# Performance work log

Measured on AMD Instinct MI355X. Metric: run time of the kernel, lower is better.

## Reference

```python
import jax, jax.numpy as jnp
import numpy as np

INPUT_DIM = 1024
UNITS = 1024

def setup_inputs() -> dict:
    key = jax.random.key(0)
    ks = jax.random.split(key, 7)
    B, S = 4, 2048
    x = jax.random.normal(ks[0], (B, S, INPUT_DIM), dtype=jnp.float32)
    # nn.Linear weights stored as [out, in]; biases [out]
    scale = 1.0 / np.sqrt(INPUT_DIM)
    Wq = jax.random.uniform(ks[1], (UNITS, INPUT_DIM), jnp.float32, -scale, scale)
    bq = jax.random.uniform(ks[2], (UNITS,), jnp.float32, -scale, scale)
    Wk = jax.random.uniform(ks[3], (UNITS, INPUT_DIM), jnp.float32, -scale, scale)
    bk = jax.random.uniform(ks[4], (UNITS,), jnp.float32, -scale, scale)
    Wv = jax.random.uniform(ks[5], (UNITS, INPUT_DIM), jnp.float32, -scale, scale)
    bv = jax.random.uniform(ks[6], (UNITS,), jnp.float32, -scale, scale)
    return {"x": x, "Wq": Wq, "bq": bq, "Wk": Wk, "bk": bk, "Wv": Wv, "bv": bv}

def reference(x, Wq, bq, Wk, bk, Wv, bv):
    # Q/K/V projections: [B,S,D] @ [D,U]
    Q = jnp.einsum('bsd,ud->bsu', x, Wq) + bq
    K = jnp.einsum('bsd,ud->bsu', x, Wk) + bk
    V = jnp.einsum('bsd,ud->bsu', x, Wv) + bv
    scores = jnp.einsum('bqu,bku->bqk', Q, K) / jnp.sqrt(jnp.float32(UNITS))
    attn = jax.nn.softmax(scores, axis=-1)
    return jnp.einsum('bqk,bku->bqu', attn, V)
```

## Files before the change

kernel.cpp:

```cpp
#include <hip/hip_runtime.h>
#include <cstdint>
#include <cstddef>


typedef unsigned short ushort_t;
typedef __attribute__((ext_vector_type(8))) short short8;
typedef __attribute__((ext_vector_type(4))) float f32x4;

#define AS1 __attribute__((address_space(1)))
#define AS3 __attribute__((address_space(3)))

__device__ __forceinline__ ushort_t f2bf(float f) {
    unsigned int u = __float_as_uint(f);
    u += 0x7FFFu + ((u >> 16) & 1u);
    return (ushort_t)(u >> 16);
}
__device__ __forceinline__ float bf2f(ushort_t b) {
    return __uint_as_float(((unsigned)b) << 16);
}

__device__ __forceinline__ void async_ld16(const void* g, unsigned lds_off) {
    __builtin_amdgcn_global_load_lds((const AS1 void*)(uintptr_t)g,
                                     (AS3 void*)(uintptr_t)lds_off,
                                     16, 0, 0);
}

template <typename OT, int EPI, int CX, int CY>
__global__ __launch_bounds__(256, 2) void gemm_db(
    const ushort_t* __restrict__ A, const ushort_t* __restrict__ B,
    const float* __restrict__ bias0, const float* __restrict__ bias1,
    OT* __restrict__ C, int K, int lda, int ldb, int ldc, float scale,
    long long aOffZ, long long bOffZ, long long cOffZ)
{
    constexpr int BK = 64;
    constexpr int NCALL = 4;

    __shared__ __align__(16) ushort_t As[2][128 * BK];
    __shared__ __align__(16) ushort_t Bs[2][128 * BK];
    __shared__ float rs[128];

    const int tid  = threadIdx.x;
    const int wave = tid >> 6;
    const int lane = tid & 63;

    const int GX  = gridDim.x, GY = gridDim.y, GZ = gridDim.z;
    const int bid = blockIdx.x + GX * (blockIdx.y + GY * blockIdx.z);
    const int xcd = bid & 7;
    const int jj  = bid >> 3;
    const int CZ  = (GX * GY * GZ) / (8 * CX * CY);
    const int NCX = GX / CX, NCY = GY / CY;
    const int cx  = xcd % NCX;
    const int ct  = xcd / NCX;
    const int cy  = ct % NCY, cz = ct / NCY;
    const int bx  = cx * CX + (jj % CX);
    const int by  = cy * CY + ((jj / CX) % CY);
    const int bz  = cz * CZ + jj / (CX * CY);

    A += (size_t)bz * aOffZ;
    B += (size_t)bz * bOffZ;

    const int m0 = by * 128;
    const int n0 = bx * 128;
    const int wm = (wave >> 1) * 64;
    const int wn = (wave & 1) * 64;

    const unsigned lw  = (unsigned)(wave << 10);
    const unsigned aL0 = (unsigned)(uintptr_t)&As[0][0] + lw;
    const unsigned aL1 = (unsigned)(uintptr_t)&As[1][0] + lw;
    const unsigned bL0 = (unsigned)(uintptr_t)&Bs[0][0] + lw;
    const unsigned bL1 = (unsigned)(uintptr_t)&Bs[1][0] + lw;

    const int srow = wave * 8 + (lane >> 3);
    const int cd   = ((lane & 7) - srow) & 7;
    const ushort_t* gA = A + (size_t)(m0 + srow) * lda + cd * 8;
    const ushort_t* gB = B + (size_t)(n0 + srow) * ldb + cd * 8;

    auto stageT = [&](int t, unsigned la, unsigned lb) {
        const ushort_t* pA = gA + (size_t)t * BK;
        const ushort_t* pB = gB + (size_t)t * BK;
#pragma unroll
        for (int c = 0; c < NCALL; ++c) {
            async_ld16(pA + (size_t)(c * 32) * lda, la + c * 4096);
            async_ld16(pB + (size_t)(c * 32) * ldb, lb + c * 4096);
        }
    };

    const int frow = lane & 15;
    const int fg   = lane >> 4;

    const int NT = K / BK;

    f32x4 acc[4][4] = {};
    float rsacc[4] = {0.f, 0.f, 0.f, 0.f};

    auto computeT = [&](const ushort_t* Aw, const ushort_t* Bw) {
#pragma unroll
        for (int t2 = 0; t2 < 2; ++t2) {
            const int pa = (((t2 << 2) + fg + frow) & 7) << 3;
            short8 af[4], bf[4];
#pragma unroll
            for (int i = 0; i < 4; ++i)
                af[i] = *(const short8*)&Aw[(wm + i * 16 + frow) * BK + pa];
            if (EPI == 4 && wn == 0) {
#pragma unroll
                for (int i = 0; i < 4; ++i)
#pragma unroll
                    for (int e = 0; e < 8; ++e)
                        rsacc[i] += bf2f((ushort_t)af[i][e]);
            }
#pragma unroll
            for (int j = 0; j < 4; ++j)
                bf[j] = *(const short8*)&Bw[(wn + j * 16 + frow) * BK + pa];
#pragma unroll
            for (int i = 0; i < 4; ++i)
#pragma unroll
                for (int j = 0; j < 4; ++j)
                    acc[i][j] = __builtin_amdgcn_mfma_f32_16x16x32_bf16(
                        af[i], bf[j], acc[i][j], 0, 0, 0);
        }
    };

    const ushort_t* A0 = &As[0][0];
    const ushort_t* A1 = &As[1][0];
    const ushort_t* B0 = &Bs[0][0];
    const ushort_t* B1 = &Bs[1][0];

    stageT(0, aL0, bL0);
    __syncthreads();

    int t = 0;
    for (; t + 2 < NT; t += 2) {
        stageT(t + 1, aL1, bL1);
        computeT(A0, B0);
        __syncthreads();
        stageT(t + 2, aL0, bL0);
        computeT(A1, B1);
        __syncthreads();
    }
    stageT(NT - 1, aL1, bL1);
    computeT(A0, B0);
    __syncthreads();
    computeT(A1, B1);

    if (EPI == 4) {
        if (wn == 0) {
#pragma unroll
            for (int i = 0; i < 4; ++i) {
                float s = rsacc[i];
                s += __shfl_xor(s, 16, 64);
                s += __shfl_xor(s, 32, 64);
                rs[wm + i * 16 + frow] = s;
            }
        }
        __syncthreads();
    }

    C += (size_t)bz * cOffZ;
    const int r0 = fg << 2;
    const int c0 = lane & 15;
#pragma unroll
    for (int i = 0; i < 4; ++i) {
        float bm[4];
        if (EPI == 2) {
#pragma unroll
            for (int r = 0; r < 4; ++r)
                bm[r] = bias0[m0 + wm + i * 16 + r0 + r];
        }
        if (EPI == 4) {
#pragma unroll
            for (int r = 0; r < 4; ++r)
                bm[r] = 1.0f / rs[wm + i * 16 + r0 + r];
        }
#pragma unroll
        for (int j = 0; j < 4; ++j) {
            const int n = n0 + wn + j * 16 + c0;
            float bn = 0.f;
            if (EPI == 1) bn = (n < 1024) ? bias0[n] : bias1[n - 1024];
#pragma unroll
            for (int r = 0; r < 4; ++r) {
                const int m = m0 + wm + i * 16 + r0 + r;
                float v = acc[i][j][r] * scale;
                if (EPI == 1) v += bn;
                if (EPI == 2) v += bm[r];
                if (EPI == 3) v = __expf(v);
                if (EPI == 4) v *= bm[r];
                if constexpr (sizeof(OT) == 2)
                    C[(size_t)m * ldc + n] = f2bf(v);
                else
                    C[(size_t)m * ldc + n] = v;
            }
        }
    }
}

__global__ __launch_bounds__(256) void cvt_all(
    const float* __restrict__ x,  const float* __restrict__ wq,
    const float* __restrict__ wk, const float* __restrict__ wv,
    ushort_t* __restrict__ xb,  ushort_t* __restrict__ wqb,
    ushort_t* __restrict__ wkb, ushort_t* __restrict__ wvb)
{
    const int b = blockIdx.x;
    const float* src; ushort_t* dst; size_t base;
    if (b < 4096)      { src = x;  dst = xb;  base = (size_t)b * 2048; }
    else if (b < 4608) { src = wq; dst = wqb; base = (size_t)(b - 4096) * 2048; }
    else if (b < 5120) { src = wk; dst = wkb; base = (size_t)(b - 4608) * 2048; }
    else               { src = wv; dst = wvb; base = (size_t)(b - 5120) * 2048; }
    const size_t i = base + threadIdx.x * 8;
    const f32x4 a = *(const f32x4*)(src + i);
    const f32x4 c = *(const f32x4*)(src + i + 4);
    short8 o;
    o[0] = (short)f2bf(a[0]); o[1] = (short)f2bf(a[1]);
    o[2] = (short)f2bf(a[2]); o[3] = (short)f2bf(a[3]);
    o[4] = (short)f2bf(c[0]); o[5] = (short)f2bf(c[1]);
    o[6] = (short)f2bf(c[2]); o[7] = (short)f2bf(c[3]);
    *(short8*)(dst + i) = o;
}

extern "C" void kernel_launch(void* const* d_in, const int* in_sizes, int n_in,
                              void* d_out, int out_size, void* d_ws, size_t ws_size,
                              hipStream_t stream)
{
    const float* x  = (const float*)d_in[0];
    const float* Wq = (const float*)d_in[1];
    const float* bq = (const float*)d_in[2];
    const float* Wk = (const float*)d_in[3];
    const float* bk = (const float*)d_in[4];
    const float* Wv = (const float*)d_in[5];
    const float* bv = (const float*)d_in[6];
    float* out = (float*)d_out;

    char* ws = (char*)d_ws;
    const size_t MB = 1ull << 20;
    ushort_t* Xb   = (ushort_t*)(ws);
    ushort_t* Wqkb = (ushort_t*)(ws + 16 * MB);
    ushort_t* Wvb  = (ushort_t*)(ws + 20 * MB);
    ushort_t* QKb  = (ushort_t*)(ws + 32 * MB);
    ushort_t* Vt   = (ushort_t*)(ws + 64 * MB);
    ushort_t* Sc   = (ushort_t*)(ws);

    cvt_all<<<dim3(5632), dim3(256), 0, stream>>>(
        x, Wq, Wk, Wv, Xb, Wqkb, (ushort_t*)(ws + 18 * MB), Wvb);

    gemm_db<ushort_t, 1, 8, 16><<<dim3(16, 64, 1), dim3(256), 0, stream>>>(
        Xb, Wqkb, bq, bk, QKb, 1024, 1024, 1024, 2048, 1.0f, 0, 0, 0);

    gemm_db<ushort_t, 2, 16, 4><<<dim3(64, 8, 1), dim3(256), 0, stream>>>(
        Wvb, Xb, bv, nullptr, Vt, 1024, 1024, 1024, 8192, 1.0f, 0, 0, 0);

    gemm_db<ushort_t, 3, 8, 16><<<dim3(16, 16, 4), dim3(256), 0, stream>>>(
        QKb, QKb + 1024, nullptr, nullptr, Sc, 1024, 2048, 2048, 2048,
        0.03125f, 2048ll * 2048, 2048ll * 2048, 2048ll * 2048);

    gemm_db<float, 4, 8, 8><<<dim3(8, 16, 4), dim3(256), 0, stream>>>(
        Sc, Vt, nullptr, nullptr, out, 2048, 2048, 8192, 1024, 1.0f,
        2048ll * 2048, 2048ll, 2048ll * 1024);
}
```

Baseline: 239.0 us.

## Merge QK and V projection GEMMs into one launch; compute row sums via MFMA

The separate QK-projection and V-projection GEMM launches become one kernel with 1536 blocks that pick their operands, XCD-aware tile mapping and bias epilogue from the block index. This removes a launch and the tail idle time between the two GEMMs. In the final PV GEMM, the per-row sum of the bf16 attention weights is now computed with an extra MFMA against a vector of ones instead of scalar bf16-to-float adds followed by shuffles. The cost is more MFMA work in wn==0 waves and a larger, branchier merged kernel. An unused remap2 helper is also added.

Measured after the change: 235.3 us. No clear change (-1.6%).

```diff
diff --git a/kernel.cpp b/kernel.cpp
--- a/kernel.cpp
+++ b/kernel.cpp
@@ -15,9 +15,6 @@
     u += 0x7FFFu + ((u >> 16) & 1u);
     return (ushort_t)(u >> 16);
 }
-__device__ __forceinline__ float bf2f(ushort_t b) {
-    return __uint_as_float(((unsigned)b) << 16);
-}
 
 __device__ __forceinline__ void async_ld16(const void* g, unsigned lds_off) {
     __builtin_amdgcn_global_load_lds((const AS1 void*)(uintptr_t)g,
@@ -25,10 +22,20 @@
                                      16, 0, 0);
 }
 
+__device__ __forceinline__ void remap2(int id, int GX, int GY, int CX, int CY,
+                                       int& bx, int& by) {
+    const int xcd = id & 7;
+    const int jj  = id >> 3;
+    const int NCX = GX / CX;
+    const int cx  = xcd % NCX;
+    const int cy  = xcd / NCX;
+    bx = cx * CX + jj % CX;
+    by = cy * CY + (jj / CX) % ((GY / CY) == 0 ? 1 : CY);
+}
+
 template <typename OT, int EPI, int CX, int CY>
 __global__ __launch_bounds__(256, 2) void gemm_db(
     const ushort_t* __restrict__ A, const ushort_t* __restrict__ B,
-    const float* __restrict__ bias0, const float* __restrict__ bias1,
     OT* __restrict__ C, int K, int lda, int ldb, int ldc, float scale,
     long long aOffZ, long long bOffZ, long long cOffZ)
 {
@@ -91,7 +98,10 @@
     const int NT = K / BK;
 
     f32x4 acc[4][4] = {};
-    float rsacc[4] = {0.f, 0.f, 0.f, 0.f};
+    f32x4 rsm[4] = {};
+    const short8 ones = { (short)0x3F80, (short)0x3F80, (short)0x3F80,
+                          (short)0x3F80, (short)0x3F80, (short)0x3F80,
+                          (short)0x3F80, (short)0x3F80 };
 
     auto computeT = [&](const ushort_t* Aw, const ushort_t* Bw) {
 #pragma unroll
@@ -104,9 +114,8 @@
             if (EPI == 4 && wn == 0) {
 #pragma unroll
                 for (int i = 0; i < 4; ++i)
-#pragma unroll
-                    for (int e = 0; e < 8; ++e)
-                        rsacc[i] += bf2f((ushort_t)af[i][e]);
+                    rsm[i] = __builtin_amdgcn_mfma_f32_16x16x32_bf16(
+                        af[i], ones, rsm[i], 0, 0, 0);
             }
 #pragma unroll
             for (int j = 0; j < 4; ++j)
@@ -142,30 +151,24 @@
     __syncthreads();
     computeT(A1, B1);
 
-    if (EPI == 4) {
-        if (wn == 0) {
-#pragma unroll
-            for (int i = 0; i < 4; ++i) {
-                float s = rsacc[i];
-                s += __shfl_xor(s, 16, 64);
-                s += __shfl_xor(s, 32, 64);
-                rs[wm + i * 16 + frow] = s;
-            }
-        }
-        __syncthreads();
-    }
-
-    C += (size_t)bz * cOffZ;
     const int r0 = fg << 2;
     const int c0 = lane & 15;
+
+    if (EPI == 4) {
+        if (wn == 0 && c0 == 0) {
+#pragma unroll
+            for (int i = 0; i < 4; ++i)
+#pragma unroll
+                for (int r = 0; r < 4; ++r)
+                    rs[wm + i * 16 + r0 + r] = rsm[i][r];
+        }
+        __syncthreads();
+    }
+
+    C += (size_t)bz * cOffZ;
 #pragma unroll
     for (int i = 0; i < 4; ++i) {
         float bm[4];
-        if (EPI == 2) {
-#pragma unroll
-            for (int r = 0; r < 4; ++r)
-                bm[r] = bias0[m0 + wm + i * 16 + r0 + r];
-        }
         if (EPI == 4) {
 #pragma unroll
             for (int r = 0; r < 4; ++r)
@@ -174,20 +177,150 @@
 #pragma unroll
         for (int j = 0; j < 4; ++j) {
             const int n = n0 + wn + j * 16 + c0;
-            float bn = 0.f;
-            if (EPI == 1) bn = (n < 1024) ? bias0[n] : bias1[n - 1024];
 #pragma unroll
             for (int r = 0; r < 4; ++r) {
                 const int m = m0 + wm + i * 16 + r0 + r;
                 float v = acc[i][j][r] * scale;
-                if (EPI == 1) v += bn;
-                if (EPI == 2) v += bm[r];
                 if (EPI == 3) v = __expf(v);
                 if (EPI == 4) v *= bm[r];
                 if constexpr (sizeof(OT) == 2)
                     C[(size_t)m * ldc + n] = f2bf(v);
                 else
                     C[(size_t)m * ldc + n] = v;
+            }
+        }
+    }
+}
+
+__global__ __launch_bounds__(256, 2) void gemm_mrg(
+    const ushort_t* __restrict__ Xb, const ushort_t* __restrict__ Wqkb,
+    const ushort_t* __restrict__ Wvb,
+    const float* __restrict__ bq, const float* __restrict__ bk,
+    const float* __restrict__ bv,
+    ushort_t* __restrict__ QKb, ushort_t* __restrict__ Vtp)
+{
+    constexpr int BK = 64;
+    constexpr int NCALL = 4;
+
+    __shared__ __align__(16) ushort_t As[2][128 * BK];
+    __shared__ __align__(16) ushort_t Bs[2][128 * BK];
+
+    const int tid  = threadIdx.x;
+    const int wave = tid >> 6;
+    const int lane = tid & 63;
+
+    const bool vtR = (blockIdx.x >= 1024);
+    const int  id  = vtR ? (int)blockIdx.x - 1024 : (int)blockIdx.x;
+
+    int bx, by;
+    if (!vtR) {
+        const int xcd = id & 7, jj = id >> 3;
+        bx = (xcd % 2) * 8  + (jj % 8);
+        by = (xcd / 2) * 16 + (jj / 8);
+    } else {
+        const int xcd = id & 7, jj = id >> 3;
+        bx = (xcd % 4) * 16 + (jj % 16);
+        by = (xcd / 4) * 4  + (jj / 16);
+    }
+
+    const ushort_t* A = vtR ? Wvb : Xb;
+    const ushort_t* B = vtR ? Xb  : Wqkb;
+    ushort_t*       C = vtR ? Vtp : QKb;
+    const int ldc = vtR ? 8192 : 2048;
+
+    const int m0 = by * 128;
+    const int n0 = bx * 128;
+    const int wm = (wave >> 1) * 64;
+    const int wn = (wave & 1) * 64;
+
+    const unsigned lw  = (unsigned)(wave << 10);
+    const unsigned aL0 = (unsigned)(uintptr_t)&As[0][0] + lw;
+    const unsigned aL1 = (unsigned)(uintptr_t)&As[1][0] + lw;
+    const unsigned bL0 = (unsigned)(uintptr_t)&Bs[0][0] + lw;
+    const unsigned bL1 = (unsigned)(uintptr_t)&Bs[1][0] + lw;
+
+    const int srow = wave * 8 + (lane >> 3);
+    const int cd   = ((lane & 7) - srow) & 7;
+    const ushort_t* gA = A + (size_t)(m0 + srow) * 1024 + cd * 8;
+    const ushort_t* gB = B + (size_t)(n0 + srow) * 1024 + cd * 8;
+
+    auto stageT = [&](int t, unsigned la, unsigned lb) {
+        const ushort_t* pA = gA + (size_t)t * BK;
+        const ushort_t* pB = gB + (size_t)t * BK;
+#pragma unroll
+        for (int c = 0; c < NCALL; ++c) {
+            async_ld16(pA + (size_t)(c * 32) * 1024, la + c * 4096);
+            async_ld16(pB + (size_t)(c * 32) * 1024, lb + c * 4096);
+        }
+    };
+
+    const int frow = lane & 15;
+    const int fg   = lane >> 4;
+
+    f32x4 acc[4][4] = {};
+
+    auto computeT = [&](const ushort_t* Aw, const ushort_t* Bw) {
+#pragma unroll
+        for (int t2 = 0; t2 < 2; ++t2) {
+            const int pa = (((t2 << 2) + fg + frow) & 7) << 3;
+            short8 af[4], bf[4];
+#pragma unroll
+            for (int i = 0; i < 4; ++i)
+                af[i] = *(const short8*)&Aw[(wm + i * 16 + frow) * BK + pa];
+#pragma unroll
+            for (int j = 0; j < 4; ++j)
+                bf[j] = *(const short8*)&Bw[(wn + j * 16 + frow) * BK + pa];
+#pragma unroll
+            for (int i = 0; i < 4; ++i)
+#pragma unroll
+                for (int j = 0; j < 4; ++j)
+                    acc[i][j] = __builtin_amdgcn_mfma_f32_16x16x32_bf16(
+                        af[i], bf[j], acc[i][j], 0, 0, 0);
+        }
+    };
+
+    const ushort_t* A0 = &As[0][0];
+    const ushort_t* A1 = &As[1][0];
+    const ushort_t* B0 = &Bs[0][0];
+    const ushort_t* B1 = &Bs[1][0];
+
+    stageT(0, aL0, bL0);
+    __syncthreads();
+
+    int t = 0;
+    for (; t + 2 < 16; t += 2) {
+        stageT(t + 1, aL1, bL1);
+        computeT(A0, B0);
+        __syncthreads();
+        stageT(t + 2, aL0, bL0);
+        computeT(A1, B1);
+        __syncthreads();
+    }
+    stageT(15, aL1, bL1);
+    computeT(A0, B0);
+    __syncthreads();
+    computeT(A1, B1);
+
+    const int r0 = fg << 2;
+    const int c0 = lane & 15;
+#pragma unroll
+    for (int i = 0; i < 4; ++i) {
+        float bm[4];
+        if (vtR) {
+#pragma unroll
+            for (int r = 0; r < 4; ++r)
+                bm[r] = bv[m0 + wm + i * 16 + r0 + r];
+        }
+#pragma unroll
+        for (int j = 0; j < 4; ++j) {
+            const int n = n0 + wn + j * 16 + c0;
+            float bn = 0.f;
+            if (!vtR) bn = (n < 1024) ? bq[n] : bk[n - 1024];
+#pragma unroll
+            for (int r = 0; r < 4; ++r) {
+                const int m = m0 + wm + i * 16 + r0 + r;
+                float v = acc[i][j][r] + (vtR ? bm[r] : bn);
+                C[(size_t)m * ldc + n] = f2bf(v);
             }
         }
     }
@@ -241,17 +374,14 @@
     cvt_all<<<dim3(5632), dim3(256), 0, stream>>>(
         x, Wq, Wk, Wv, Xb, Wqkb, (ushort_t*)(ws + 18 * MB), Wvb);
 
-    gemm_db<ushort_t, 1, 8, 16><<<dim3(16, 64, 1), dim3(256), 0, stream>>>(
-        Xb, Wqkb, bq, bk, QKb, 1024, 1024, 1024, 2048, 1.0f, 0, 0, 0);
-
-    gemm_db<ushort_t, 2, 16, 4><<<dim3(64, 8, 1), dim3(256), 0, stream>>>(
-        Wvb, Xb, bv, nullptr, Vt, 1024, 1024, 1024, 8192, 1.0f, 0, 0, 0);
+    gemm_mrg<<<dim3(1536), dim3(256), 0, stream>>>(
+        Xb, Wqkb, Wvb, bq, bk, bv, QKb, Vt);
 
     gemm_db<ushort_t, 3, 8, 16><<<dim3(16, 16, 4), dim3(256), 0, stream>>>(
-        QKb, QKb + 1024, nullptr, nullptr, Sc, 1024, 2048, 2048, 2048,
+        QKb, QKb + 1024, Sc, 1024, 2048, 2048, 2048,
         0.03125f, 2048ll * 2048, 2048ll * 2048, 2048ll * 2048);
 
     gemm_db<float, 4, 8, 8><<<dim3(8, 16, 4), dim3(256), 0, stream>>>(
-        Sc, Vt, nullptr, nullptr, out, 2048, 2048, 8192, 1024, 1.0f,
+        Sc, Vt, out, 2048, 2048, 8192, 1024, 1.0f,
         2048ll * 2048, 2048ll, 2048ll * 1024);
 }
```

## Fuse pipeline into cooperative persistent megakernel with grid syncs

Applied to the files above, without the earlier changes.

Replaces the separate cast and GEMM launches with one cooperative persistent kernel that loops over work units and uses grid-wide syncs between stages. This removes per-launch gaps and tail effects. The fallback path merges the QK and V projection GEMMs into a single launch. The softmax row-sum is now computed with an MFMA against a ones vector instead of scalar adds. Risks include grid.sync overhead and the fixed 512-block grid underfilling or imbalancing work across stages.

After: 218.9 us. 1.09x faster.

```diff
diff --git a/kernel.cpp b/kernel.cpp
--- a/kernel.cpp
+++ b/kernel.cpp
@@ -1,6 +1,9 @@
 #include <hip/hip_runtime.h>
+#include <hip/hip_cooperative_groups.h>
 #include <cstdint>
 #include <cstddef>
+
+namespace cg = cooperative_groups;
 
 
 typedef unsigned short ushort_t;
@@ -15,9 +18,6 @@
     u += 0x7FFFu + ((u >> 16) & 1u);
     return (ushort_t)(u >> 16);
 }
-__device__ __forceinline__ float bf2f(ushort_t b) {
-    return __uint_as_float(((unsigned)b) << 16);
-}
 
 __device__ __forceinline__ void async_ld16(const void* g, unsigned lds_off) {
     __builtin_amdgcn_global_load_lds((const AS1 void*)(uintptr_t)g,
@@ -25,42 +25,30 @@
                                      16, 0, 0);
 }
 
-template <typename OT, int EPI, int CX, int CY>
-__global__ __launch_bounds__(256, 2) void gemm_db(
+template <int GX, int GY, int GZ, int CX, int CY>
+__device__ __forceinline__ void remapC(int id, int& bx, int& by, int& bz) {
+    constexpr int CZ  = (GX * GY * GZ) / (8 * CX * CY);
+    constexpr int NCX = GX / CX, NCY = GY / CY;
+    const int xcd = id & 7, jj = id >> 3;
+    const int cx = xcd % NCX, ct = xcd / NCX;
+    const int cy = ct % NCY, cz = ct / NCY;
+    bx = cx * CX + (jj % CX);
+    by = cy * CY + ((jj / CX) % CY);
+    bz = cz * CZ + jj / (CX * CY);
+}
+
+template <typename OT, int EPI>
+__device__ __forceinline__ void gemm_unit(
+    ushort_t (&As)[2][8192], ushort_t (&Bs)[2][8192], float (&rs)[128],
     const ushort_t* __restrict__ A, const ushort_t* __restrict__ B,
-    const float* __restrict__ bias0, const float* __restrict__ bias1,
-    OT* __restrict__ C, int K, int lda, int ldb, int ldc, float scale,
-    long long aOffZ, long long bOffZ, long long cOffZ)
+    const float* __restrict__ b0, const float* __restrict__ b1,
+    OT* __restrict__ C, int NT, int lda, int ldb, int ldc, float scale,
+    int m0, int n0)
 {
     constexpr int BK = 64;
-    constexpr int NCALL = 4;
-
-    __shared__ __align__(16) ushort_t As[2][128 * BK];
-    __shared__ __align__(16) ushort_t Bs[2][128 * BK];
-    __shared__ float rs[128];
-
     const int tid  = threadIdx.x;
     const int wave = tid >> 6;
     const int lane = tid & 63;
-
-    const int GX  = gridDim.x, GY = gridDim.y, GZ = gridDim.z;
-    const int bid = blockIdx.x + GX * (blockIdx.y + GY * blockIdx.z);
-    const int xcd = bid & 7;
-    const int jj  = bid >> 3;
-    const int CZ  = (GX * GY * GZ) / (8 * CX * CY);
-    const int NCX = GX / CX, NCY = GY / CY;
-    const int cx  = xcd % NCX;
-    const int ct  = xcd / NCX;
-    const int cy  = ct % NCY, cz = ct / NCY;
-    const int bx  = cx * CX + (jj % CX);
-    const int by  = cy * CY + ((jj / CX) % CY);
-    const int bz  = cz * CZ + jj / (CX * CY);
-
-    A += (size_t)bz * aOffZ;
-    B += (size_t)bz * bOffZ;
-
-    const int m0 = by * 128;
-    const int n0 = bx * 128;
     const int wm = (wave >> 1) * 64;
     const int wn = (wave & 1) * 64;
 
@@ -79,7 +67,7 @@
         const ushort_t* pA = gA + (size_t)t * BK;
         const ushort_t* pB = gB + (size_t)t * BK;
 #pragma unroll
-        for (int c = 0; c < NCALL; ++c) {
+        for (int c = 0; c < 4; ++c) {
             async_ld16(pA + (size_t)(c * 32) * lda, la + c * 4096);
             async_ld16(pB + (size_t)(c * 32) * ldb, lb + c * 4096);
         }
@@ -88,10 +76,11 @@
     const int frow = lane & 15;
     const int fg   = lane >> 4;
 
-    const int NT = K / BK;
-
     f32x4 acc[4][4] = {};
-    float rsacc[4] = {0.f, 0.f, 0.f, 0.f};
+    f32x4 rsm[4] = {};
+    const short8 ones = { (short)0x3F80, (short)0x3F80, (short)0x3F80,
+                          (short)0x3F80, (short)0x3F80, (short)0x3F80,
+                          (short)0x3F80, (short)0x3F80 };
 
     auto computeT = [&](const ushort_t* Aw, const ushort_t* Bw) {
 #pragma unroll
@@ -104,9 +93,8 @@
             if (EPI == 4 && wn == 0) {
 #pragma unroll
                 for (int i = 0; i < 4; ++i)
-#pragma unroll
-                    for (int e = 0; e < 8; ++e)
-                        rsacc[i] += bf2f((ushort_t)af[i][e]);
+                    rsm[i] = __builtin_amdgcn_mfma_f32_16x16x32_bf16(
+                        af[i], ones, rsm[i], 0, 0, 0);
             }
 #pragma unroll
             for (int j = 0; j < 4; ++j)
@@ -142,29 +130,27 @@
     __syncthreads();
     computeT(A1, B1);
 
-    if (EPI == 4) {
-        if (wn == 0) {
-#pragma unroll
-            for (int i = 0; i < 4; ++i) {
-                float s = rsacc[i];
-                s += __shfl_xor(s, 16, 64);
-                s += __shfl_xor(s, 32, 64);
-                rs[wm + i * 16 + frow] = s;
-            }
-        }
-        __syncthreads();
-    }
-
-    C += (size_t)bz * cOffZ;
     const int r0 = fg << 2;
     const int c0 = lane & 15;
+
+    if (EPI == 4) {
+        if (wn == 0 && c0 == 0) {
+#pragma unroll
+            for (int i = 0; i < 4; ++i)
+#pragma unroll
+                for (int r = 0; r < 4; ++r)
+                    rs[wm + i * 16 + r0 + r] = rsm[i][r];
+        }
+        __syncthreads();
+    }
+
 #pragma unroll
     for (int i = 0; i < 4; ++i) {
         float bm[4];
         if (EPI == 2) {
 #pragma unroll
             for (int r = 0; r < 4; ++r)
-                bm[r] = bias0[m0 + wm + i * 16 + r0 + r];
+                bm[r] = b0[m0 + wm + i * 16 + r0 + r];
         }
         if (EPI == 4) {
 #pragma unroll
@@ -175,7 +161,7 @@
         for (int j = 0; j < 4; ++j) {
             const int n = n0 + wn + j * 16 + c0;
             float bn = 0.f;
-            if (EPI == 1) bn = (n < 1024) ? bias0[n] : bias1[n - 1024];
+            if (EPI == 1) bn = (n < 1024) ? b0[n] : b1[n - 1024];
 #pragma unroll
             for (int r = 0; r < 4; ++r) {
                 const int m = m0 + wm + i * 16 + r0 + r;
@@ -193,18 +179,15 @@
     }
 }
 
-__global__ __launch_bounds__(256) void cvt_all(
-    const float* __restrict__ x,  const float* __restrict__ wq,
-    const float* __restrict__ wk, const float* __restrict__ wv,
-    ushort_t* __restrict__ xb,  ushort_t* __restrict__ wqb,
-    ushort_t* __restrict__ wkb, ushort_t* __restrict__ wvb)
-{
-    const int b = blockIdx.x;
+__device__ __forceinline__ void cast_unit(
+    int u, const float* x, const float* Wq, const float* Wk, const float* Wv,
+    ushort_t* Xb, ushort_t* Wqkb, ushort_t* Wkb, ushort_t* Wvb)
+{
     const float* src; ushort_t* dst; size_t base;
-    if (b < 4096)      { src = x;  dst = xb;  base = (size_t)b * 2048; }
-    else if (b < 4608) { src = wq; dst = wqb; base = (size_t)(b - 4096) * 2048; }
-    else if (b < 5120) { src = wk; dst = wkb; base = (size_t)(b - 4608) * 2048; }
-    else               { src = wv; dst = wvb; base = (size_t)(b - 5120) * 2048; }
+    if (u < 4096)      { src = x;  dst = Xb;   base = (size_t)u * 2048; }
+    else if (u < 4608) { src = Wq; dst = Wqkb; base = (size_t)(u - 4096) * 2048; }
+    else if (u < 5120) { src = Wk; dst = Wkb;  base = (size_t)(u - 4608) * 2048; }
+    else               { src = Wv; dst = Wvb;  base = (size_t)(u - 5120) * 2048; }
     const size_t i = base + threadIdx.x * 8;
     const f32x4 a = *(const f32x4*)(src + i);
     const f32x4 c = *(const f32x4*)(src + i + 4);
@@ -216,6 +199,140 @@
     *(short8*)(dst + i) = o;
 }
 
+__global__ __launch_bounds__(256, 2) void mega(
+    const float* __restrict__ x,
+    const float* __restrict__ Wq, const float* __restrict__ bq,
+    const float* __restrict__ Wk, const float* __restrict__ bk,
+    const float* __restrict__ Wv, const float* __restrict__ bv,
+    float* __restrict__ out, char* __restrict__ ws)
+{
+    __shared__ __align__(16) ushort_t As[2][8192];
+    __shared__ __align__(16) ushort_t Bs[2][8192];
+    __shared__ float rs[128];
+
+    const size_t MB = 1ull << 20;
+    ushort_t* Xb   = (ushort_t*)(ws);
+    ushort_t* Wqkb = (ushort_t*)(ws + 16 * MB);
+    ushort_t* Wkb  = (ushort_t*)(ws + 18 * MB);
+    ushort_t* Wvb  = (ushort_t*)(ws + 20 * MB);
+    ushort_t* QKb  = (ushort_t*)(ws + 32 * MB);
+    ushort_t* Vt   = (ushort_t*)(ws + 64 * MB);
+    ushort_t* Sc   = (ushort_t*)(ws);
+    float* outp = out;
+
+    cg::grid_group grid = cg::this_grid();
+    const int gb = blockIdx.x;
+    const int GS = gridDim.x;
+
+    for (int u = gb; u < 5632; u += GS)
+        cast_unit(u, x, Wq, Wk, Wv, Xb, Wqkb, Wkb, Wvb);
+    grid.sync();
+
+    for (int u = gb; u < 1536; u += GS) {
+        int bx, by, bz;
+        if (u < 1024) {
+            remapC<16, 64, 1, 8, 16>(u, bx, by, bz);
+            gemm_unit<ushort_t, 1>(As, Bs, rs, Xb, Wqkb, bq, bk,
+                                   QKb, 16, 1024, 1024, 2048, 1.0f,
+                                   by * 128, bx * 128);
+        } else {
+            remapC<64, 8, 1, 16, 4>(u - 1024, bx, by, bz);
+            gemm_unit<ushort_t, 2>(As, Bs, rs, Wvb, Xb, bv, nullptr,
+                                   Vt, 16, 1024, 1024, 8192, 1.0f,
+                                   by * 128, bx * 128);
+        }
+        __syncthreads();
+    }
+    grid.sync();
+
+    for (int u = gb; u < 1024; u += GS) {
+        int bx, by, bz;
+        remapC<16, 16, 4, 8, 16>(u, bx, by, bz);
+        const size_t zo = (size_t)bz * 2048 * 2048;
+        gemm_unit<ushort_t, 3>(As, Bs, rs, QKb + zo, QKb + 1024 + zo,
+                               nullptr, nullptr,
+                               Sc + zo, 16, 2048, 2048, 2048, 0.03125f,
+                               by * 128, bx * 128);
+        __syncthreads();
+    }
+    grid.sync();
+
+    for (int u = gb; u < 512; u += GS) {
+        int bx, by, bz;
+        remapC<8, 16, 4, 8, 8>(u, bx, by, bz);
+        gemm_unit<float, 4>(As, Bs, rs,
+                            Sc + (size_t)bz * 2048 * 2048,
+                            Vt + (size_t)bz * 2048,
+                            nullptr, nullptr,
+                            outp + (size_t)bz * 2048 * 1024,
+                            32, 2048, 8192, 1024, 1.0f,
+                            by * 128, bx * 128);
+        __syncthreads();
+    }
+}
+
+template <typename OT, int EPI, int CX, int CY>
+__global__ __launch_bounds__(256, 2) void gemm_db(
+    const ushort_t* __restrict__ A, const ushort_t* __restrict__ B,
+    OT* __restrict__ C, int NT, int lda, int ldb, int ldc, float scale,
+    long long aOffZ, long long bOffZ, long long cOffZ)
+{
+    __shared__ __align__(16) ushort_t As[2][8192];
+    __shared__ __align__(16) ushort_t Bs[2][8192];
+    __shared__ float rs[128];
+
+    const int GX  = gridDim.x, GY = gridDim.y, GZ = gridDim.z;
+    const int bid = blockIdx.x + GX * (blockIdx.y + GY * blockIdx.z);
+    const int xcd = bid & 7, jj = bid >> 3;
+    const int CZ  = (GX * GY * GZ) / (8 * CX * CY);
+    const int NCX = GX / CX, NCY = GY / CY;
+    const int cx  = xcd % NCX, ct = xcd / NCX;
+    const int cy  = ct % NCY, cz = ct / NCY;
+    const int bx  = cx * CX + (jj % CX);
+    const int by  = cy * CY + ((jj / CX) % CY);
+    const int bz  = cz * CZ + jj / (CX * CY);
+
+    gemm_unit<OT, EPI>(As, Bs, rs,
+                       A + (size_t)bz * aOffZ, B + (size_t)bz * bOffZ,
+                       nullptr, nullptr,
+                       C + (size_t)bz * cOffZ, NT, lda, ldb, ldc, scale,
+                       by * 128, bx * 128);
+}
+
+__global__ __launch_bounds__(256, 2) void gemm_mrg(
+    const ushort_t* __restrict__ Xb, const ushort_t* __restrict__ Wqkb,
+    const ushort_t* __restrict__ Wvb,
+    const float* __restrict__ bq, const float* __restrict__ bk,
+    const float* __restrict__ bv,
+    ushort_t* __restrict__ QKb, ushort_t* __restrict__ Vtp)
+{
+    __shared__ __align__(16) ushort_t As[2][8192];
+    __shared__ __align__(16) ushort_t Bs[2][8192];
+    __shared__ float rs[128];
+
+    int bx, by, bz;
+    if (blockIdx.x < 1024) {
+        remapC<16, 64, 1, 8, 16>((int)blockIdx.x, bx, by, bz);
+        gemm_unit<ushort_t, 1>(As, Bs, rs, Xb, Wqkb, bq, bk,
+                               QKb, 16, 1024, 1024, 2048, 1.0f,
+                               by * 128, bx * 128);
+    } else {
+        remapC<64, 8, 1, 16, 4>((int)blockIdx.x - 1024, bx, by, bz);
+        gemm_unit<ushort_t, 2>(As, Bs, rs, Wvb, Xb, bv, nullptr,
+                               Vtp, 16, 1024, 1024, 8192, 1.0f,
+                               by * 128, bx * 128);
+    }
+}
+
+__global__ __launch_bounds__(256) void cvt_all(
+    const float* __restrict__ x,  const float* __restrict__ wq,
+    const float* __restrict__ wk, const float* __restrict__ wv,
+    ushort_t* __restrict__ xb,  ushort_t* __restrict__ wqb,
+    ushort_t* __restrict__ wkb, ushort_t* __restrict__ wvb)
+{
+    cast_unit((int)blockIdx.x, x, wq, wk, wv, xb, wqb, wkb, wvb);
+}
+
 extern "C" void kernel_launch(void* const* d_in, const int* in_sizes, int n_in,
                               void* d_out, int out_size, void* d_ws, size_t ws_size,
                               hipStream_t stream)
@@ -228,8 +345,21 @@
     const float* Wv = (const float*)d_in[5];
     const float* bv = (const float*)d_in[6];
     float* out = (float*)d_out;
-
     char* ws = (char*)d_ws;
+
+    int nb = 0;
+    hipError_t qe = hipOccupancyMaxActiveBlocksPerMultiprocessor(
+        &nb, reinterpret_cast<const void*>(mega), 256, 0);
+    if (qe == hipSuccess && nb >= 2) {
+        void* args[] = { (void*)&x, (void*)&Wq, (void*)&bq, (void*)&Wk,
+                         (void*)&bk, (void*)&Wv, (void*)&bv, (void*)&out,
+                         (void*)&ws };
+        hipError_t le = hipLaunchCooperativeKernel(
+            reinterpret_cast<const void*>(mega), dim3(512), dim3(256),
+            args, 0, stream);
+        if (le == hipSuccess) return;
+    }
+
     const size_t MB = 1ull << 20;
     ushort_t* Xb   = (ushort_t*)(ws);
     ushort_t* Wqkb = (ushort_t*)(ws + 16 * MB);
@@ -241,17 +371,14 @@
     cvt_all<<<dim3(5632), dim3(256), 0, stream>>>(
         x, Wq, Wk, Wv, Xb, Wqkb, (ushort_t*)(ws + 18 * MB), Wvb);
 
-    gemm_db<ushort_t, 1, 8, 16><<<dim3(16, 64, 1), dim3(256), 0, stream>>>(
-        Xb, Wqkb, bq, bk, QKb, 1024, 1024, 1024, 2048, 1.0f, 0, 0, 0);
-
-    gemm_db<ushort_t, 2, 16, 4><<<dim3(64, 8, 1), dim3(256), 0, stream>>>(
-        Wvb, Xb, bv, nullptr, Vt, 1024, 1024, 1024, 8192, 1.0f, 0, 0, 0);
+    gemm_mrg<<<dim3(1536), dim3(256), 0, stream>>>(
+        Xb, Wqkb, Wvb, bq, bk, bv, QKb, Vt);
 
     gemm_db<ushort_t, 3, 8, 16><<<dim3(16, 16, 4), dim3(256), 0, stream>>>(
-        QKb, QKb + 1024, nullptr, nullptr, Sc, 1024, 2048, 2048, 2048,
+        QKb, QKb + 1024, Sc, 16, 2048, 2048, 2048,
         0.03125f, 2048ll * 2048, 2048ll * 2048, 2048ll * 2048);
 
     gemm_db<float, 4, 8, 8><<<dim3(8, 16, 4), dim3(256), 0, stream>>>(
-        Sc, Vt, nullptr, nullptr, out, 2048, 2048, 8192, 1024, 1.0f,
+        Sc, Vt, out, 32, 2048, 8192, 1024, 1.0f,
         2048ll * 2048, 2048ll, 2048ll * 1024);
 }
```
